# Kernel optimization log

Measured on AMD Instinct MI355X. Metric: run time of the kernel, lower is better.

## Reference

```python
import jax, jax.numpy as jnp
import numpy as np


def setup_inputs() -> dict:
    key = jax.random.key(0)
    ks = jax.random.split(key, 5)
    B, T, D, U = 32, 2048, 512, 512
    scale = 1.0 / np.sqrt(D)
    return {
        "full": jax.random.normal(ks[0], (B, T, D), jnp.float32),
        "last": jax.random.normal(ks[1], (B, D), jnp.float32),
        "W1": jax.random.normal(ks[2], (D, U), jnp.float32) * scale,
        "b1": jnp.zeros((U,), jnp.float32),
        "W2": jax.random.normal(ks[3], (D, U), jnp.float32) * scale,
        "b2": jnp.zeros((U,), jnp.float32),
        "V": jax.random.normal(ks[4], (U, 1), jnp.float32) * (1.0 / np.sqrt(U)),
        "bV": jnp.zeros((1,), jnp.float32),
    }


def reference(full, last, W1, b1, W2, b2, V, bV):
    # full: [B,T,D], last: [B,D]
    h1 = jnp.einsum("btd,du->btu", full, W1) + b1          # [B,T,U]
    h2 = last @ W2 + b2                                      # [B,U]
    score = jnp.tanh(h1 + h2[:, None, :]) @ V + bV           # [B,T,1]
    attn = jax.nn.softmax(score, axis=1)                     # [B,T,1]
    context = jnp.sum(attn * full, axis=1)                   # [B,D]
    return context
```

## Files before the change

kernel.cpp:

```cpp
#include <hip/hip_runtime.h>
#include <math.h>


#define BB 32
#define TT 2048
#define DD 512
#define UU 512

typedef short bf16x8 __attribute__((ext_vector_type(8)));
typedef float f32x4  __attribute__((ext_vector_type(4)));

static __device__ __forceinline__ short f2bf(float f) {
    unsigned x = __float_as_uint(f);
    return (short)((x + 0x7fffu + ((x >> 16) & 1u)) >> 16);
}

static __device__ __forceinline__ float fast_tanh(float x) {
    float e = __expf(2.f * x);
    return 1.f - 2.f * __builtin_amdgcn_rcpf(e + 1.f);
}

__global__ __launch_bounds__(256) void prep_kernel(const float* __restrict__ W1,
                                                   short* __restrict__ W1T,
                                                   const float* __restrict__ last,
                                                   const float* __restrict__ W2,
                                                   const float* __restrict__ b1,
                                                   const float* __restrict__ b2,
                                                   float* __restrict__ h2,
                                                   float* __restrict__ scores,
                                                   float* __restrict__ out) {
    __shared__ float tile[32][33];
    __shared__ float ls[DD];
    __shared__ float part[256];
    const int bid = blockIdx.x;
    const int tid = threadIdx.x;
    if (bid < 256) {
        const int tr = (bid >> 4) << 5;
        const int tc = (bid & 15) << 5;
#pragma unroll
        for (int p = 0; p < 4; ++p) {
            const int r = p * 8 + (tid >> 5), c = tid & 31;
            tile[r][c] = W1[(size_t)(tr + r) * UU + tc + c];
        }
        __syncthreads();
#pragma unroll
        for (int p = 0; p < 4; ++p) {
            const int r = p * 8 + (tid >> 5), c = tid & 31;
            W1T[(size_t)(tc + r) * DD + tr + c] = f2bf(tile[c][r]);
        }
    } else if (bid < 384) {
        const int b2i = bid - 256;
        const int b  = b2i >> 2;
        const int u0 = (b2i & 3) << 7;
        for (int i = tid; i < DD; i += 256) ls[i] = last[b * DD + i];
        __syncthreads();
        const int uu = tid & 127;
        const int dh = tid >> 7;
        float acc = 0.f;
#pragma unroll 8
        for (int d = dh * 256; d < dh * 256 + 256; ++d)
            acc += ls[d] * W2[d * UU + u0 + uu];
        part[tid] = acc;
        __syncthreads();
        if (tid < 128) {
            const int u = u0 + tid;
            h2[b * UU + u] = part[tid] + part[tid + 128] + b1[u] + b2[u];
        }
    } else if (bid == 384) {
        float4 z = make_float4(0.f, 0.f, 0.f, 0.f);
        for (int i = tid; i < (BB * TT) / 4; i += 256) ((float4*)scores)[i] = z;
    } else {
        float4 z = make_float4(0.f, 0.f, 0.f, 0.f);
        for (int i = tid; i < (BB * DD) / 4; i += 256) ((float4*)out)[i] = z;
    }
}

__global__ __launch_bounds__(256, 2) void score_kernel(const float* __restrict__ full,
                                                       const short* __restrict__ W1T,
                                                       const float* __restrict__ h2,
                                                       const float* __restrict__ V,
                                                       float* __restrict__ scores) {
    __shared__ __align__(16) float a32[64 * 32];
    __shared__ __align__(16) short blds[256 * 32];
    __shared__ float score_red[4][64];

    const int bid = blockIdx.x;
    const int b  = bid >> 6;
    const int t0 = ((bid >> 1) & 31) << 6;
    const int u0 = (bid & 1) << 8;
    const int tid = threadIdx.x;
    const int w    = tid >> 6;
    const int lane = tid & 63;
    const int quad = lane >> 4;
    const int col  = lane & 15;

    f32x4 acc[4][4];
#pragma unroll
    for (int i = 0; i < 4; ++i)
#pragma unroll
        for (int j = 0; j < 4; ++j) acc[i][j] = (f32x4){0.f, 0.f, 0.f, 0.f};

    const size_t fullbase = (size_t)(b * TT + t0) * DD;

    for (int ko = 0; ko < 16; ++ko) {
        if (ko) __syncthreads();
#pragma unroll
        for (int i = 0; i < 2; ++i) {
            const int id = w * 128 + i * 64 + lane;
            const int r  = id >> 3;
            const int cc = (id & 7) ^ (r & 7);
            const float* g = &full[fullbase + (size_t)r * DD + ko * 32 + cc * 4];
            __builtin_amdgcn_global_load_lds(
                (const __attribute__((address_space(1))) void*)g,
                (__attribute__((address_space(3))) void*)&a32[(w * 128 + i * 64) * 4],
                16, 0, 0);
        }
#pragma unroll
        for (int i = 0; i < 4; ++i) {
            const int id = w * 256 + i * 64 + lane;
            const int ul = id >> 2;
            const int kc = (id & 3) ^ (ul & 3) ^ ((ul >> 2) & 3);
            const short* g = &W1T[(size_t)(u0 + ul) * DD + ko * 32 + kc * 8];
            __builtin_amdgcn_global_load_lds(
                (const __attribute__((address_space(1))) void*)g,
                (__attribute__((address_space(3))) void*)&blds[(w * 256 + i * 64) * 8],
                16, 0, 0);
        }
        __syncthreads();

        bf16x8 af[4];
#pragma unroll
        for (int mt = 0; mt < 4; ++mt) {
            const int r = mt * 16 + col;
            const f32x4 lo = *(const f32x4*)&a32[(r * 8 + ((quad * 2 + 0) ^ (r & 7))) * 4];
            const f32x4 hi = *(const f32x4*)&a32[(r * 8 + ((quad * 2 + 1) ^ (r & 7))) * 4];
            af[mt] = (bf16x8){f2bf(lo.x), f2bf(lo.y), f2bf(lo.z), f2bf(lo.w),
                              f2bf(hi.x), f2bf(hi.y), f2bf(hi.z), f2bf(hi.w)};
        }
#pragma unroll
        for (int nt = 0; nt < 4; ++nt) {
            const int ul = w * 64 + nt * 16 + col;
            const int sl = ul * 4 + (quad ^ (ul & 3) ^ ((ul >> 2) & 3));
            const bf16x8 bf = *(const bf16x8*)&blds[sl * 8];
#pragma unroll
            for (int mt = 0; mt < 4; ++mt)
                acc[mt][nt] = __builtin_amdgcn_mfma_f32_16x16x32_bf16(af[mt], bf, acc[mt][nt], 0, 0, 0);
        }
    }

    float srow[16];
#pragma unroll
    for (int i = 0; i < 16; ++i) srow[i] = 0.f;
#pragma unroll
    for (int nt = 0; nt < 4; ++nt) {
        const int u = u0 + w * 64 + nt * 16 + col;
        const float hv = h2[b * UU + u];
        const float vv = V[u];
#pragma unroll
        for (int mt = 0; mt < 4; ++mt)
#pragma unroll
            for (int r = 0; r < 4; ++r)
                srow[mt * 4 + r] += fast_tanh(acc[mt][nt][r] + hv) * vv;
    }
#pragma unroll
    for (int off = 1; off < 16; off <<= 1) {
#pragma unroll
        for (int i = 0; i < 16; ++i) srow[i] += __shfl_xor(srow[i], off, 64);
    }
    if (col == 0) {
#pragma unroll
        for (int mt = 0; mt < 4; ++mt)
#pragma unroll
            for (int r = 0; r < 4; ++r)
                score_red[w][mt * 16 + quad * 4 + r] = srow[mt * 4 + r];
    }
    __syncthreads();
    if (tid < 64)
        atomicAdd(&scores[b * TT + t0 + tid],
                  score_red[0][tid] + score_red[1][tid] + score_red[2][tid] + score_red[3][tid]);
}

__global__ __launch_bounds__(256) void context_kernel(const float* __restrict__ full,
                                                      const float* __restrict__ scores,
                                                      float* __restrict__ out) {
    const int bid = blockIdx.x;
    const int b  = bid >> 4;
    const int d0 = ((bid >> 2) & 3) << 7;
    const int t0 = (bid & 3) << 9;
    const int tid = threadIdx.x;
    const int c  = tid & 31;
    const int tr = tid >> 5;

    __shared__ float red[256];
    __shared__ float ps[512];
    __shared__ float4 red4[256];

    float local[8];
    float m = -1e30f;
#pragma unroll
    for (int j = 0; j < 8; ++j) {
        local[j] = scores[b * TT + j * 256 + tid];
        m = fmaxf(m, local[j]);
    }
    red[tid] = m;
    __syncthreads();
    for (int s = 128; s > 0; s >>= 1) {
        if (tid < s) red[tid] = fmaxf(red[tid], red[tid + s]);
        __syncthreads();
    }
    const float mx = red[0];
    __syncthreads();

    float sum = 0.f;
    float e[8];
#pragma unroll
    for (int j = 0; j < 8; ++j) {
        e[j] = __expf(local[j] - mx);
        sum += e[j];
    }
    const int jb = (bid & 3) * 2;
#pragma unroll
    for (int i = 0; i < 2; ++i) ps[i * 256 + tid] = e[jb + i];
    red[tid] = sum;
    __syncthreads();
    for (int s = 128; s > 0; s >>= 1) {
        if (tid < s) red[tid] += red[tid + s];
        __syncthreads();
    }
    const float inv = 1.f / red[0];

    float ax = 0.f, ay = 0.f, az = 0.f, aw = 0.f;
    const float* base = full + ((size_t)(b * TT + t0)) * DD + d0;
#pragma unroll 4
    for (int it = 0; it < 64; ++it) {
        const int t = it * 8 + tr;
        const float4 v = *(const float4*)&base[(size_t)t * DD + c * 4];
        const float wg = ps[t];
        ax += wg * v.x; ay += wg * v.y; az += wg * v.z; aw += wg * v.w;
    }
    red4[tid] = make_float4(ax, ay, az, aw);
    __syncthreads();
    if (tid < 32) {
        float4 s = red4[tid];
#pragma unroll
        for (int g = 1; g < 8; ++g) {
            const float4 o = red4[g * 32 + tid];
            s.x += o.x; s.y += o.y; s.z += o.z; s.w += o.w;
        }
        atomicAdd(&out[b * DD + d0 + tid * 4 + 0], s.x * inv);
        atomicAdd(&out[b * DD + d0 + tid * 4 + 1], s.y * inv);
        atomicAdd(&out[b * DD + d0 + tid * 4 + 2], s.z * inv);
        atomicAdd(&out[b * DD + d0 + tid * 4 + 3], s.w * inv);
    }
}

extern "C" void kernel_launch(void* const* d_in, const int* in_sizes, int n_in,
                              void* d_out, int out_size, void* d_ws, size_t ws_size,
                              hipStream_t stream) {
    const float* full = (const float*)d_in[0];
    const float* last = (const float*)d_in[1];
    const float* W1   = (const float*)d_in[2];
    const float* b1   = (const float*)d_in[3];
    const float* W2   = (const float*)d_in[4];
    const float* b2   = (const float*)d_in[5];
    const float* V    = (const float*)d_in[6];

    float* out    = (float*)d_out;
    float* scores = (float*)d_ws;
    float* h2     = (float*)d_ws + (size_t)BB * TT;
    short* W1T    = (short*)(h2 + (size_t)BB * UU);

    prep_kernel<<<386, 256, 0, stream>>>(W1, W1T, last, W2, b1, b2, h2, scores, out);
    score_kernel<<<BB * (TT / 64) * 2, 256, 0, stream>>>(full, W1T, h2, V, scores);
    context_kernel<<<512, 256, 0, stream>>>(full, scores, out);
}
```

Measured before the change: 293.2 us.

## Fuse softmax and context into score kernel with flash-style split-T combine

Each block now computes all 512 U columns for a 128-row T tile, so the per-tile score is complete without atomics. Inside the block it applies a local softmax (max and sum of exponentials) and accumulates the weighted context over the same tile, which should be cache-hot. A small combine kernel then merges the per-tile partials using the saved max and sum. This removes the separate context pass, the zeroing of scores and output, and the atomics. The cost is a larger block (512 threads, bigger LDS and accumulator footprint), which may lower occupancy and leaves only 512 blocks.

```diff
diff --git a/kernel.cpp b/kernel.cpp
--- a/kernel.cpp
+++ b/kernel.cpp
@@ -26,9 +26,7 @@
                                                    const float* __restrict__ W2,
                                                    const float* __restrict__ b1,
                                                    const float* __restrict__ b2,
-                                                   float* __restrict__ h2,
-                                                   float* __restrict__ scores,
-                                                   float* __restrict__ out) {
+                                                   float* __restrict__ h2) {
     __shared__ float tile[32][33];
     __shared__ float ls[DD];
     __shared__ float part[256];
@@ -48,7 +46,7 @@
             const int r = p * 8 + (tid >> 5), c = tid & 31;
             W1T[(size_t)(tc + r) * DD + tr + c] = f2bf(tile[c][r]);
         }
-    } else if (bid < 384) {
+    } else {
         const int b2i = bid - 256;
         const int b  = b2i >> 2;
         const int u0 = (b2i & 3) << 7;
@@ -66,85 +64,89 @@
             const int u = u0 + tid;
             h2[b * UU + u] = part[tid] + part[tid + 128] + b1[u] + b2[u];
         }
-    } else if (bid == 384) {
-        float4 z = make_float4(0.f, 0.f, 0.f, 0.f);
-        for (int i = tid; i < (BB * TT) / 4; i += 256) ((float4*)scores)[i] = z;
-    } else {
-        float4 z = make_float4(0.f, 0.f, 0.f, 0.f);
-        for (int i = tid; i < (BB * DD) / 4; i += 256) ((float4*)out)[i] = z;
-    }
-}
-
-__global__ __launch_bounds__(256, 2) void score_kernel(const float* __restrict__ full,
-                                                       const short* __restrict__ W1T,
-                                                       const float* __restrict__ h2,
-                                                       const float* __restrict__ V,
-                                                       float* __restrict__ scores) {
-    __shared__ __align__(16) float a32[64 * 32];
-    __shared__ __align__(16) short blds[256 * 32];
-    __shared__ float score_red[4][64];
+    }
+}
+
+__global__ __launch_bounds__(512) void score_kernel(const float* __restrict__ full,
+                                                    const short* __restrict__ W1T,
+                                                    const float* __restrict__ h2,
+                                                    const float* __restrict__ V,
+                                                    float* __restrict__ ctx,
+                                                    float* __restrict__ m_arr,
+                                                    float* __restrict__ l_arr) {
+    __shared__ __align__(16) float a32[128 * 64];
+    __shared__ __align__(16) short blds[512 * 64];
+    __shared__ float red64[8][64];
+    __shared__ float esc[128];
+    __shared__ float sred[8];
+    __shared__ __align__(16) float red4[4][128][4];
 
     const int bid = blockIdx.x;
-    const int b  = bid >> 6;
-    const int t0 = ((bid >> 1) & 31) << 6;
-    const int u0 = (bid & 1) << 8;
-    const int tid = threadIdx.x;
+    const int b    = bid >> 4;
+    const int t0   = (bid & 15) << 7;
+    const int tid  = threadIdx.x;
     const int w    = tid >> 6;
     const int lane = tid & 63;
     const int quad = lane >> 4;
     const int col  = lane & 15;
-
-    f32x4 acc[4][4];
+    const int wm   = w >> 2;
+    const int wn   = w & 3;
+
+    f32x4 acc[4][8];
 #pragma unroll
     for (int i = 0; i < 4; ++i)
 #pragma unroll
-        for (int j = 0; j < 4; ++j) acc[i][j] = (f32x4){0.f, 0.f, 0.f, 0.f};
+        for (int j = 0; j < 8; ++j) acc[i][j] = (f32x4){0.f, 0.f, 0.f, 0.f};
 
     const size_t fullbase = (size_t)(b * TT + t0) * DD;
 
-    for (int ko = 0; ko < 16; ++ko) {
+    for (int ko = 0; ko < 8; ++ko) {
         if (ko) __syncthreads();
 #pragma unroll
-        for (int i = 0; i < 2; ++i) {
-            const int id = w * 128 + i * 64 + lane;
-            const int r  = id >> 3;
-            const int cc = (id & 7) ^ (r & 7);
-            const float* g = &full[fullbase + (size_t)r * DD + ko * 32 + cc * 4];
+        for (int i = 0; i < 4; ++i) {
+            const int sb = w * 256 + i * 64;
+            const int s  = sb + lane;
+            const int r  = s >> 4;
+            const int cc = (s & 15) ^ (r & 15);
+            const float* g = &full[fullbase + (size_t)r * DD + ko * 64 + cc * 4];
             __builtin_amdgcn_global_load_lds(
                 (const __attribute__((address_space(1))) void*)g,
-                (__attribute__((address_space(3))) void*)&a32[(w * 128 + i * 64) * 4],
-                16, 0, 0);
-        }
-#pragma unroll
-        for (int i = 0; i < 4; ++i) {
-            const int id = w * 256 + i * 64 + lane;
-            const int ul = id >> 2;
-            const int kc = (id & 3) ^ (ul & 3) ^ ((ul >> 2) & 3);
-            const short* g = &W1T[(size_t)(u0 + ul) * DD + ko * 32 + kc * 8];
+                (__attribute__((address_space(3))) void*)&a32[sb * 4], 16, 0, 0);
+        }
+#pragma unroll
+        for (int i = 0; i < 8; ++i) {
+            const int sb = w * 512 + i * 64;
+            const int s  = sb + lane;
+            const int u  = s >> 3;
+            const int kc = (s & 7) ^ (u & 7);
+            const short* g = &W1T[(size_t)u * DD + ko * 64 + kc * 8];
             __builtin_amdgcn_global_load_lds(
                 (const __attribute__((address_space(1))) void*)g,
-                (__attribute__((address_space(3))) void*)&blds[(w * 256 + i * 64) * 8],
-                16, 0, 0);
-        }
-        __syncthreads();
-
-        bf16x8 af[4];
-#pragma unroll
-        for (int mt = 0; mt < 4; ++mt) {
-            const int r = mt * 16 + col;
-            const f32x4 lo = *(const f32x4*)&a32[(r * 8 + ((quad * 2 + 0) ^ (r & 7))) * 4];
-            const f32x4 hi = *(const f32x4*)&a32[(r * 8 + ((quad * 2 + 1) ^ (r & 7))) * 4];
-            af[mt] = (bf16x8){f2bf(lo.x), f2bf(lo.y), f2bf(lo.z), f2bf(lo.w),
-                              f2bf(hi.x), f2bf(hi.y), f2bf(hi.z), f2bf(hi.w)};
-        }
-#pragma unroll
-        for (int nt = 0; nt < 4; ++nt) {
-            const int ul = w * 64 + nt * 16 + col;
-            const int sl = ul * 4 + (quad ^ (ul & 3) ^ ((ul >> 2) & 3));
-            const bf16x8 bf = *(const bf16x8*)&blds[sl * 8];
-#pragma unroll
-            for (int mt = 0; mt < 4; ++mt)
-                acc[mt][nt] = __builtin_amdgcn_mfma_f32_16x16x32_bf16(af[mt], bf, acc[mt][nt], 0, 0, 0);
+                (__attribute__((address_space(3))) void*)&blds[sb * 8], 16, 0, 0);
+        }
+        __syncthreads();
+
+#pragma unroll
+        for (int ki = 0; ki < 2; ++ki) {
+            bf16x8 af[4];
+#pragma unroll
+            for (int mt = 0; mt < 4; ++mt) {
+                const int r   = wm * 64 + mt * 16 + col;
+                const int cc0 = ki * 8 + quad * 2;
+                const f32x4 lo = *(const f32x4*)&a32[(r * 16 + (cc0 ^ (r & 15))) * 4];
+                const f32x4 hi = *(const f32x4*)&a32[(r * 16 + ((cc0 + 1) ^ (r & 15))) * 4];
+                af[mt] = (bf16x8){f2bf(lo.x), f2bf(lo.y), f2bf(lo.z), f2bf(lo.w),
+                                  f2bf(hi.x), f2bf(hi.y), f2bf(hi.z), f2bf(hi.w)};
+            }
+#pragma unroll
+            for (int nt = 0; nt < 8; ++nt) {
+                const int u  = wn * 128 + nt * 16 + col;
+                const int kc = ki * 4 + quad;
+                const bf16x8 bf = *(const bf16x8*)&blds[(u * 8 + (kc ^ (u & 7))) * 8];
+#pragma unroll
+                for (int mt = 0; mt < 4; ++mt)
+                    acc[mt][nt] = __builtin_amdgcn_mfma_f32_16x16x32_bf16(af[mt], bf, acc[mt][nt], 0, 0, 0);
+            }
         }
     }
 
@@ -152,8 +154,8 @@
 #pragma unroll
     for (int i = 0; i < 16; ++i) srow[i] = 0.f;
 #pragma unroll
-    for (int nt = 0; nt < 4; ++nt) {
-        const int u = u0 + w * 64 + nt * 16 + col;
+    for (int nt = 0; nt < 8; ++nt) {
+        const int u = wn * 128 + nt * 16 + col;
         const float hv = h2[b * UU + u];
         const float vv = V[u];
 #pragma unroll
@@ -172,86 +174,88 @@
         for (int mt = 0; mt < 4; ++mt)
 #pragma unroll
             for (int r = 0; r < 4; ++r)
-                score_red[w][mt * 16 + quad * 4 + r] = srow[mt * 4 + r];
-    }
-    __syncthreads();
-    if (tid < 64)
-        atomicAdd(&scores[b * TT + t0 + tid],
-                  score_red[0][tid] + score_red[1][tid] + score_red[2][tid] + score_red[3][tid]);
-}
-
-__global__ __launch_bounds__(256) void context_kernel(const float* __restrict__ full,
-                                                      const float* __restrict__ scores,
+                red64[w][mt * 16 + quad * 4 + r] = srow[mt * 4 + r];
+    }
+    __syncthreads();
+
+    float sv = 0.f;
+    if (tid < 128) {
+        const int wmX = tid >> 6, rr = tid & 63;
+        sv = red64[wmX * 4 + 0][rr] + red64[wmX * 4 + 1][rr] +
+             red64[wmX * 4 + 2][rr] + red64[wmX * 4 + 3][rr];
+        float mv = sv;
+#pragma unroll
+        for (int off = 1; off < 64; off <<= 1) mv = fmaxf(mv, __shfl_xor(mv, off, 64));
+        if (lane == 0) sred[w] = mv;
+    }
+    __syncthreads();
+    const float M = fmaxf(sred[0], sred[1]);
+    if (tid < 128) {
+        float e = __expf(sv - M);
+        esc[tid] = e;
+#pragma unroll
+        for (int off = 1; off < 64; off <<= 1) e += __shfl_xor(e, off, 64);
+        if (lane == 0) sred[4 + w] = e;
+    }
+    __syncthreads();
+    if (tid == 0) { m_arr[bid] = M; l_arr[bid] = sred[4] + sred[5]; }
+
+    const int c  = tid & 127;
+    const int tp = tid >> 7;
+    float ax = 0.f, ay = 0.f, az = 0.f, aw = 0.f;
+#pragma unroll 4
+    for (int i = 0; i < 32; ++i) {
+        const int t = i * 4 + tp;
+        const float4 v = *(const float4*)&full[fullbase + (size_t)t * DD + c * 4];
+        const float e = esc[t];
+        ax += e * v.x; ay += e * v.y; az += e * v.z; aw += e * v.w;
+    }
+    *(float4*)&red4[tp][c][0] = make_float4(ax, ay, az, aw);
+    __syncthreads();
+    if (tp == 0) {
+        const float4 p0 = *(const float4*)&red4[0][c][0];
+        const float4 p1 = *(const float4*)&red4[1][c][0];
+        const float4 p2 = *(const float4*)&red4[2][c][0];
+        const float4 p3 = *(const float4*)&red4[3][c][0];
+        float4 s = make_float4(p0.x + p1.x + p2.x + p3.x,
+                               p0.y + p1.y + p2.y + p3.y,
+                               p0.z + p1.z + p2.z + p3.z,
+                               p0.w + p1.w + p2.w + p3.w);
+        *(float4*)&ctx[(size_t)bid * DD + c * 4] = s;
+    }
+}
+
+__global__ __launch_bounds__(256) void combine_kernel(const float* __restrict__ ctx,
+                                                      const float* __restrict__ m_arr,
+                                                      const float* __restrict__ l_arr,
                                                       float* __restrict__ out) {
-    const int bid = blockIdx.x;
-    const int b  = bid >> 4;
-    const int d0 = ((bid >> 2) & 3) << 7;
-    const int t0 = (bid & 3) << 9;
+    const int b = blockIdx.x;
     const int tid = threadIdx.x;
-    const int c  = tid & 31;
-    const int tr = tid >> 5;
-
-    __shared__ float red[256];
-    __shared__ float ps[512];
-    __shared__ float4 red4[256];
-
-    float local[8];
-    float m = -1e30f;
-#pragma unroll
-    for (int j = 0; j < 8; ++j) {
-        local[j] = scores[b * TT + j * 256 + tid];
-        m = fmaxf(m, local[j]);
-    }
-    red[tid] = m;
-    __syncthreads();
-    for (int s = 128; s > 0; s >>= 1) {
-        if (tid < s) red[tid] = fmaxf(red[tid], red[tid + s]);
-        __syncthreads();
-    }
-    const float mx = red[0];
-    __syncthreads();
-
-    float sum = 0.f;
-    float e[8];
-#pragma unroll
-    for (int j = 0; j < 8; ++j) {
-        e[j] = __expf(local[j] - mx);
-        sum += e[j];
-    }
-    const int jb = (bid & 3) * 2;
-#pragma unroll
-    for (int i = 0; i < 2; ++i) ps[i * 256 + tid] = e[jb + i];
-    red[tid] = sum;
-    __syncthreads();
-    for (int s = 128; s > 0; s >>= 1) {
-        if (tid < s) red[tid] += red[tid + s];
-        __syncthreads();
-    }
-    const float inv = 1.f / red[0];
-
-    float ax = 0.f, ay = 0.f, az = 0.f, aw = 0.f;
-    const float* base = full + ((size_t)(b * TT + t0)) * DD + d0;
-#pragma unroll 4
-    for (int it = 0; it < 64; ++it) {
-        const int t = it * 8 + tr;
-        const float4 v = *(const float4*)&base[(size_t)t * DD + c * 4];
-        const float wg = ps[t];
-        ax += wg * v.x; ay += wg * v.y; az += wg * v.z; aw += wg * v.w;
-    }
-    red4[tid] = make_float4(ax, ay, az, aw);
-    __syncthreads();
-    if (tid < 32) {
-        float4 s = red4[tid];
-#pragma unroll
-        for (int g = 1; g < 8; ++g) {
-            const float4 o = red4[g * 32 + tid];
-            s.x += o.x; s.y += o.y; s.z += o.z; s.w += o.w;
-        }
-        atomicAdd(&out[b * DD + d0 + tid * 4 + 0], s.x * inv);
-        atomicAdd(&out[b * DD + d0 + tid * 4 + 1], s.y * inv);
-        atomicAdd(&out[b * DD + d0 + tid * 4 + 2], s.z * inv);
-        atomicAdd(&out[b * DD + d0 + tid * 4 + 3], s.w * inv);
-    }
+    __shared__ float wgt[16];
+    __shared__ float linv;
+    if (tid == 0) {
+        float M = -1e30f;
+#pragma unroll
+        for (int i = 0; i < 16; ++i) M = fmaxf(M, m_arr[b * 16 + i]);
+        float l = 0.f;
+#pragma unroll
+        for (int i = 0; i < 16; ++i) {
+            wgt[i] = __expf(m_arr[b * 16 + i] - M);
+            l += wgt[i] * l_arr[b * 16 + i];
+        }
+        linv = 1.f / l;
+    }
+    __syncthreads();
+    float s0 = 0.f, s1 = 0.f;
+#pragma unroll
+    for (int i = 0; i < 16; ++i) {
+        const float wi = wgt[i];
+        const float* cp = &ctx[(size_t)(b * 16 + i) * DD + tid * 2];
+        s0 += wi * cp[0];
+        s1 += wi * cp[1];
+    }
+    out[b * DD + tid * 2]     = s0 * linv;
+    out[b * DD + tid * 2 + 1] = s1 * linv;
 }
 
 extern "C" void kernel_launch(void* const* d_in, const int* in_sizes, int n_in,
@@ -265,12 +269,14 @@
     const float* b2   = (const float*)d_in[5];
     const float* V    = (const float*)d_in[6];
 
-    float* out    = (float*)d_out;
-    float* scores = (float*)d_ws;
-    float* h2     = (float*)d_ws + (size_t)BB * TT;
-    short* W1T    = (short*)(h2 + (size_t)BB * UU);
-
-    prep_kernel<<<386, 256, 0, stream>>>(W1, W1T, last, W2, b1, b2, h2, scores, out);
-    score_kernel<<<BB * (TT / 64) * 2, 256, 0, stream>>>(full, W1T, h2, V, scores);
-    context_kernel<<<512, 256, 0, stream>>>(full, scores, out);
-}
+    float* out   = (float*)d_out;
+    float* h2    = (float*)d_ws;
+    float* m_arr = h2 + (size_t)BB * UU;
+    float* l_arr = m_arr + 512;
+    float* ctx   = l_arr + 512;
+    short* W1T   = (short*)(ctx + (size_t)BB * 16 * DD);
+
+    prep_kernel<<<384, 256, 0, stream>>>(W1, W1T, last, W2, b1, b2, h2);
+    score_kernel<<<BB * 16, 512, 0, stream>>>(full, W1T, h2, V, ctx, m_arr, l_arr);
+    combine_kernel<<<BB, 256, 0, stream>>>(ctx, m_arr, l_arr, out);
+}
```

Result: faster. 270.0 us (-7.9%).
